# Optimization experiments

Hardware: AMD Instinct MI355X
Metric: run time of the kernel (lower is better)

Reference implementation:

```python
import jax, jax.numpy as jnp
import numpy as np

B, N, FIN = 64, 128, 768
NFEAT, NHID, NHEADS, NCLASS = 1024, 512, 8, 512
ALPHA = 0.2
NEG_E = -9e15
NEG_S = -9e10


def setup_inputs():
    rng = np.random.RandomState(0)
    x = rng.randn(B, N, FIN).astype(np.float32)
    offset_mapping = np.zeros((B, N, 2), dtype=np.int32)
    attention_mask = np.zeros((B, N), dtype=np.float32)
    tag = np.zeros((B, N), dtype=np.float32)
    for b in range(B):
        pos, k, groups = 1, 0, 0
        n_words = int(rng.randint(30, 60))
        for _ in range(n_words):
            wl = int(rng.randint(1, 4))
            if k + wl > 120:
                break
            for _t in range(wl):
                offset_mapping[b, k] = (pos, pos + 2)  # contiguous inside word
                pos += 2
                k += 1
            pos += 1  # 1-char gap => word boundary: end == next_start - 1
            groups += 1
        groups -= 1  # last word is never closed (matches torch loop semantics)
        attention_mask[b, :groups] = 1.0
        tag[b, :groups] = (rng.rand(groups) > 0.1).astype(np.float32)
        tag[b, 0] = 1.0
    adj = (rng.rand(B, N, N) < 0.3).astype(np.float32)
    adj = np.clip(adj + np.eye(N, dtype=np.float32)[None], 0.0, 1.0)
    s = 0.02
    p = {
        'Wg_w': s * rng.randn(FIN, NFEAT), 'Wg_b': np.zeros(NFEAT),
        'hW_w': s * rng.randn(NHEADS, NFEAT, NHID), 'hW_b': np.zeros((NHEADS, NHID)),
        'ha_w': s * rng.randn(NHEADS, 2 * NHID), 'ha_b': np.zeros(NHEADS),
        'oW_w': s * rng.randn(NHID * NHEADS, NCLASS), 'oW_b': np.zeros(NCLASS),
        'oa_w': s * rng.randn(2 * NCLASS), 'oa_b': np.zeros(()),
        'fin_w': s * rng.randn(NCLASS, 1), 'fin_b': np.zeros(1),
    }
    inp = {
        'x': jnp.asarray(x), 'tag': jnp.asarray(tag),
        'offset_mapping': jnp.asarray(offset_mapping),
        'attention_mask': jnp.asarray(attention_mask), 'adj': jnp.asarray(adj),
    }
    for kk, vv in p.items():
        inp[kk] = jnp.asarray(np.asarray(vv, dtype=np.float32))
    return inp


def _group_pool(x, offs):
    # Vectorized form of the offset-grouped mean pooling loop.
    zero = (offs[:, :, 0] == 0) & (offs[:, :, 1] == 0)  # padding rows
    fz = jnp.argmax(zero, axis=1)                       # first padding row (break)
    pos = jnp.arange(N)
    valid = pos[None, :] < fz[:, None]
    nxt_start = jnp.concatenate([offs[:, 1:, 0], jnp.zeros((offs.shape[0], 1), offs.dtype)], axis=1)
    boundary = valid & (offs[:, :, 1] == nxt_start - 1)
    bi = boundary.astype(jnp.int32)
    cs = jnp.cumsum(bi, axis=1)
    seg = cs - bi                 # exclusive cumsum: group id per token
    G = cs[:, -1]                 # number of closed groups per row

    def per(xb, segb, bb):
        sums = jax.ops.segment_sum(xb, segb, num_segments=N + 1)[:N]
        cnts = jax.ops.segment_sum(jnp.ones((N,), xb.dtype), segb, num_segments=N + 1)[:N]
        ends = jax.ops.segment_sum((jnp.arange(N) + 1) * bb, segb, num_segments=N + 1)[:N]
        return sums, cnts, ends

    sums, cnts, ends = jax.vmap(per)(x, seg, bi)
    g = jnp.arange(N)[None, :]
    gv = g < G[:, None]
    x_off = jnp.where(gv[..., None], sums / jnp.maximum(cnts, 1.0)[..., None], 0.0)
    starts = jnp.concatenate([jnp.zeros((offs.shape[0], 1), jnp.int32), ends[:, :-1]], axis=1)
    starts = jnp.where(gv, starts, 0)
    ends = jnp.where(gv, ends, 0)
    return x_off, jnp.stack([starts, ends], axis=-1)  # [B,N,F_in], [B,N,2]


def _expand_row(fix):
    # Flatten [start,end) ranges in order until the first [0,0] row; rest = arange.
    zr = (fix[:, 0] == 0) & (fix[:, 1] == 0)
    fz = jnp.argmax(zr)
    valid = jnp.arange(N) < fz
    lens = jnp.where(valid, fix[:, 1] - fix[:, 0], 0)
    csum = jnp.cumsum(lens)
    excl = csum - lens
    total = csum[-1]
    l = jnp.arange(N)
    k = jnp.clip(jnp.searchsorted(csum, l, side='right'), 0, N - 1)
    val = fix[k, 0] + (l - excl[k])
    return jnp.where(l < total, val, l)


def _scores(x_off, tag, attention_mask, adj, Wg_w, Wg_b, hW_w, hW_b, ha_w, ha_b, oW_w, oW_b, oa_w, oa_b, fin_w, fin_b):
    xw = x_off @ Wg_w + Wg_b                                    # [B,N,NFEAT]
    h = jnp.einsum('bnf,hfo->bhno', xw, hW_w) + hW_b[None, :, None, :]
    # e_ij = leakyrelu(a1.h_i + a2.h_j + b): decomposition of a([h_i||h_j])
    e = jax.nn.leaky_relu(
        jnp.einsum('bhno,ho->bhn', h, ha_w[:, :NHID])[:, :, :, None]
        + jnp.einsum('bhno,ho->bhn', h, ha_w[:, NHID:])[:, :, None, :]
        + ha_b[None, :, None, None], ALPHA)
    att = jax.nn.softmax(jnp.where(adj[:, None, :, :] > 0, e, NEG_E), axis=-1)
    x1 = jax.nn.elu(jnp.einsum('bhij,bhjo->bhio', att, h))
    x1 = x1.transpose(0, 2, 1, 3).reshape(x1.shape[0], N, NHEADS * NHID)
    h2 = x1 @ oW_w + oW_b
    e2 = jax.nn.leaky_relu((h2 @ oa_w[:NCLASS])[:, :, None]
                           + (h2 @ oa_w[NCLASS:])[:, None, :] + oa_b, ALPHA)
    att2 = jax.nn.softmax(jnp.where(adj > 0, e2, NEG_E), axis=-1)
    x2 = jax.nn.elu(jnp.einsum('bij,bjo->bio', att2, h2))
    logits = (x2 @ fin_w + fin_b)[..., 0]                        # [B,N]
    m = jnp.where(tag > 0, attention_mask, 0.0)
    sc = jax.nn.softmax(jnp.where(m > 0, logits * m, NEG_S), axis=1)
    summary = m.sum(axis=1)
    ii = (jnp.arange(N, 0, -1).astype(jnp.float32)[None, :] / summary[:, None]) * m
    ii = jax.nn.softmax(jnp.where(m > 0, ii, NEG_S), axis=1)
    return sc + ii


def reference(x, tag, offset_mapping, attention_mask, adj, Wg_w, Wg_b, hW_w, hW_b, ha_w, ha_b, oW_w, oW_b, oa_w, oa_b, fin_w, fin_b):
    x_off, index_group = _group_pool(x, offset_mapping)
    sc = _scores(x_off, tag, attention_mask, adj, Wg_w, Wg_b, hW_w, hW_b, ha_w, ha_b, oW_w, oW_b, oa_w, oa_b, fin_w, fin_b)
    order = jnp.argsort(-sc, axis=1)  # jax argsort is stable; matches torch stable descending
    bidx = jnp.arange(sc.shape[0])[:, None]
    fix = index_group.at[bidx, order].set(index_group)  # scatter_(dim=1) with permutation index
    return jax.vmap(_expand_row)(fix)
```

## Files before the change

kernel.cpp:

```cpp
#include <hip/hip_runtime.h>
#include <cstddef>
#include <cstdint>

#define B_ 64
#define N_ 128
#define FIN_ 768
#define NEG_E_ (-9.0e15f)
#define NEG_S_ (-9.0e10f)
#define CHUNK_ 16

typedef unsigned short u16;
typedef unsigned int u32;
typedef float f32x4 __attribute__((ext_vector_type(4)));
typedef short s16x8 __attribute__((ext_vector_type(8)));
typedef u16 u16x4 __attribute__((ext_vector_type(4)));
typedef u16 u16x2 __attribute__((ext_vector_type(2)));

__device__ __forceinline__ u16 f2bf(float x) {
  u32 u = __float_as_uint(x);
  return (u16)((u + 0x7fffu + ((u >> 16) & 1u)) >> 16);
}
__device__ __forceinline__ float b2f(u16 h) {
  return __uint_as_float(((u32)h) << 16);
}

__global__ __launch_bounds__(256) void group_pool_kernel(
    const float* __restrict__ x, const int* __restrict__ offs,
    u16* __restrict__ xoh, u16* __restrict__ xol, int* __restrict__ ig)
{
  const int b = blockIdx.x;
  const int fc = blockIdx.y;
  const int tid = threadIdx.x;
  __shared__ int o0[N_ + 1], o1[N_];
  __shared__ int bi[N_], cs[N_];
  __shared__ int st[N_], en[N_];
  __shared__ float invlen[N_];
  __shared__ int fzs;

  if (tid < N_) {
    o0[tid] = offs[(b * N_ + tid) * 2 + 0];
    o1[tid] = offs[(b * N_ + tid) * 2 + 1];
  }
  if (tid == 0) { o0[N_] = 0; fzs = N_; }
  __syncthreads();
  if (tid < N_ && o0[tid] == 0 && o1[tid] == 0) atomicMin(&fzs, tid);
  __syncthreads();
  const int fz = fzs;
  if (tid < N_) {
    int nxt = o0[tid + 1];
    bi[tid] = (tid < fz && o1[tid] == nxt - 1) ? 1 : 0;
    cs[tid] = bi[tid];
  }
  __syncthreads();
  for (int d = 1; d < N_; d <<= 1) {
    int v = 0;
    if (tid < N_ && tid >= d) v = cs[tid - d];
    __syncthreads();
    if (tid < N_) cs[tid] += v;
    __syncthreads();
  }
  if (tid < N_ && bi[tid]) en[cs[tid] - 1] = tid + 1;
  __syncthreads();
  const int G = cs[N_ - 1];
  if (tid < G) {
    int s = tid ? en[tid - 1] : 0;
    st[tid] = s;
    invlen[tid] = 1.0f / (float)(en[tid] - s);
  }
  __syncthreads();
  if (fc == 0 && tid < N_) {
    int g = tid;
    ig[(b * N_ + g) * 2 + 0] = (g < G) ? st[g] : 0;
    ig[(b * N_ + g) * 2 + 1] = (g < G) ? en[g] : 0;
  }

  const int f = fc * 128 + (tid & 63) * 2;
  const float* xb = x + (size_t)b * N_ * FIN_ + f;
  for (int g = tid >> 6; g < N_; g += 4) {
    u16 h0 = 0, h1 = 0, l0 = 0, l1 = 0;
    if (g < G) {
      int s = st[g], e = en[g];
      float s0 = 0.0f, s1 = 0.0f;
      for (int k = s; k < e; ++k) {
        float2 v = *(const float2*)(xb + (size_t)k * FIN_);
        s0 += v.x; s1 += v.y;
      }
      float il = invlen[g];
      float m0 = s0 * il, m1 = s1 * il;
      h0 = f2bf(m0); l0 = f2bf(m0 - b2f(h0));
      h1 = f2bf(m1); l1 = f2bf(m1 - b2f(h1));
    }
    size_t oo = ((size_t)b * N_ + g) * FIN_ + f;
    u16x2 hv = {h0, h1}, lv = {l0, l1};
    *(u16x2*)(xoh + oo) = hv;
    *(u16x2*)(xol + oo) = lv;
  }
}

__global__ __launch_bounds__(256) void pack_wgT(
    const float* __restrict__ w, u16* __restrict__ th, u16* __restrict__ tl)
{
  __shared__ float t[32][33];
  const int k0 = blockIdx.x * 32, n0 = blockIdx.y * 32;
  const int r = threadIdx.x >> 3;
  const int c = (threadIdx.x & 7) * 4;
  float4 v = *(const float4*)(w + (size_t)(k0 + r) * 1024 + n0 + c);
  t[r][c] = v.x; t[r][c + 1] = v.y; t[r][c + 2] = v.z; t[r][c + 3] = v.w;
  __syncthreads();
  u16x4 hv, lv;
#pragma unroll
  for (int i = 0; i < 4; ++i) {
    float xv = t[c + i][r];
    u16 h = f2bf(xv);
    hv[i] = h; lv[i] = f2bf(xv - b2f(h));
  }
  size_t dst = (size_t)(n0 + r) * 768 + k0 + c;
  *(u16x4*)(th + dst) = hv;
  *(u16x4*)(tl + dst) = lv;
}
__global__ __launch_bounds__(256) void pack_hwT(
    const float* __restrict__ w, u16* __restrict__ th, u16* __restrict__ tl)
{
  __shared__ float t[32][33];
  const int o0 = blockIdx.x * 32, f0 = blockIdx.y * 32, hd = blockIdx.z;
  const int r = threadIdx.x >> 3;
  const int c = (threadIdx.x & 7) * 4;
  float4 v = *(const float4*)(w + ((size_t)hd * 1024 + f0 + r) * 512 + o0 + c);
  t[r][c] = v.x; t[r][c + 1] = v.y; t[r][c + 2] = v.z; t[r][c + 3] = v.w;
  __syncthreads();
  u16x4 hv, lv;
#pragma unroll
  for (int i = 0; i < 4; ++i) {
    float xv = t[c + i][r];
    u16 h = f2bf(xv);
    hv[i] = h; lv[i] = f2bf(xv - b2f(h));
  }
  size_t dst = ((size_t)hd * 512 + o0 + r) * 1024 + f0 + c;
  *(u16x4*)(th + dst) = hv;
  *(u16x4*)(tl + dst) = lv;
}
__global__ __launch_bounds__(256) void pack_owT(
    const float* __restrict__ w, u16* __restrict__ th, u16* __restrict__ tl)
{
  __shared__ float t[32][33];
  const int k0 = blockIdx.x * 32, o0 = blockIdx.y * 32;
  const int r = threadIdx.x >> 3;
  const int c = (threadIdx.x & 7) * 4;
  float4 v = *(const float4*)(w + (size_t)(k0 + r) * 512 + o0 + c);
  t[r][c] = v.x; t[r][c + 1] = v.y; t[r][c + 2] = v.z; t[r][c + 3] = v.w;
  __syncthreads();
  u16x4 hv, lv;
#pragma unroll
  for (int i = 0; i < 4; ++i) {
    float xv = t[c + i][r];
    u16 h = f2bf(xv);
    hv[i] = h; lv[i] = f2bf(xv - b2f(h));
  }
  size_t dst = (size_t)(o0 + r) * 4096 + k0 + c;
  *(u16x4*)(th + dst) = hv;
  *(u16x4*)(tl + dst) = lv;
}

__global__ __launch_bounds__(256) void mfma_split_gemm(
    const u16* __restrict__ Ah, const u16* __restrict__ Al,
    const u16* __restrict__ Bh, const u16* __restrict__ Bl,
    const float* __restrict__ bias, int bias_mode,
    u16* __restrict__ Oh, u16* __restrict__ Ol, float* __restrict__ Of,
    int out_f32, int do_elu,
    int K, int lda, int ldb,
    long long Az, long long Bz,
    int msh, long long s_mb, int nsh, long long s_nb, long long s_n,
    long long zb_s, long long zh_s, int zH)
{
  __shared__ u16 As_h[128][40];
  __shared__ u16 As_l[128][40];
  __shared__ u16 Bs_h[128][40];
  __shared__ u16 Bs_l[128][40];
  const int tid = threadIdx.x;
  const int wave = tid >> 6, lane = tid & 63;
  const int wm = (wave >> 1) * 64, wn = (wave & 1) * 64;
  const int bn = blockIdx.x * 128, bm = blockIdx.y * 128;
  const int z = blockIdx.z;
  const u16* Ahb = Ah + (long long)z * Az;
  const u16* Alb = Al + (long long)z * Az;
  const u16* Bhb = Bh + (long long)z * Bz;
  const u16* Blb = Bl + (long long)z * Bz;
  const int lm = lane & 15, lq = lane >> 4;

  const int sr = tid >> 1;
  const int sc = (tid & 1) * 16;
  const size_t ga = (size_t)(bm + sr) * lda + sc;
  const size_t gb = (size_t)(bn + sr) * ldb + sc;

  f32x4 acc[4][4];
#pragma unroll
  for (int i = 0; i < 4; ++i)
#pragma unroll
    for (int j = 0; j < 4; ++j) acc[i][j] = (f32x4){0.0f, 0.0f, 0.0f, 0.0f};

  uint4 r0, r1, r2, r3, r4, r5, r6, r7;
  r0 = *(const uint4*)(Ahb + ga);
  r1 = *(const uint4*)(Ahb + ga + 8);
  r2 = *(const uint4*)(Alb + ga);
  r3 = *(const uint4*)(Alb + ga + 8);
  r4 = *(const uint4*)(Bhb + gb);
  r5 = *(const uint4*)(Bhb + gb + 8);
  r6 = *(const uint4*)(Blb + gb);
  r7 = *(const uint4*)(Blb + gb + 8);

  for (int k0 = 0; k0 < K; k0 += 32) {
    __syncthreads();
    *(uint4*)&As_h[sr][sc] = r0;
    *(uint4*)&As_h[sr][sc + 8] = r1;
    *(uint4*)&As_l[sr][sc] = r2;
    *(uint4*)&As_l[sr][sc + 8] = r3;
    *(uint4*)&Bs_h[sr][sc] = r4;
    *(uint4*)&Bs_h[sr][sc + 8] = r5;
    *(uint4*)&Bs_l[sr][sc] = r6;
    *(uint4*)&Bs_l[sr][sc + 8] = r7;
    __syncthreads();
    int kn = k0 + 32;
    if (kn < K) {
      r0 = *(const uint4*)(Ahb + ga + kn);
      r1 = *(const uint4*)(Ahb + ga + kn + 8);
      r2 = *(const uint4*)(Alb + ga + kn);
      r3 = *(const uint4*)(Alb + ga + kn + 8);
      r4 = *(const uint4*)(Bhb + gb + kn);
      r5 = *(const uint4*)(Bhb + gb + kn + 8);
      r6 = *(const uint4*)(Blb + gb + kn);
      r7 = *(const uint4*)(Blb + gb + kn + 8);
    }
    s16x8 fa_h[4], fa_l[4], fb_h[4], fb_l[4];
#pragma unroll
    for (int t = 0; t < 4; ++t) {
      fa_h[t] = *(const s16x8*)&As_h[wm + t * 16 + lm][lq * 8];
      fa_l[t] = *(const s16x8*)&As_l[wm + t * 16 + lm][lq * 8];
      fb_h[t] = *(const s16x8*)&Bs_h[wn + t * 16 + lm][lq * 8];
      fb_l[t] = *(const s16x8*)&Bs_l[wn + t * 16 + lm][lq * 8];
    }
#pragma unroll
    for (int i = 0; i < 4; ++i)
#pragma unroll
      for (int j = 0; j < 4; ++j) {
        acc[i][j] = __builtin_amdgcn_mfma_f32_16x16x32_bf16(fa_h[i], fb_h[j], acc[i][j], 0, 0, 0);
        acc[i][j] = __builtin_amdgcn_mfma_f32_16x16x32_bf16(fa_h[i], fb_l[j], acc[i][j], 0, 0, 0);
        acc[i][j] = __builtin_amdgcn_mfma_f32_16x16x32_bf16(fa_l[i], fb_h[j], acc[i][j], 0, 0, 0);
      }
  }

  __syncthreads();
  const long long zoff = (long long)(z / zH) * zb_s + (long long)(z % zH) * zh_s;
  const int mmask = (1 << msh) - 1;
  const int nmask = (1 << nsh) - 1;
  char* lds_raw = (char*)&As_h[0][0] + wave * 4608;
  const int rn = lane >> 2;
  const int rm = (lane & 3) * 16;

  if (out_f32) {
    float* slab = (float*)lds_raw;
#pragma unroll
    for (int j = 0; j < 4; ++j) {
#pragma unroll
      for (int i = 0; i < 4; ++i) {
        int mb = bm + wm + i * 16 + lq * 4;
        int n = bn + wn + j * 16 + lm;
        f32x4 v = acc[i][j];
        if (bias_mode == 1) v += bias[n];
        else if (bias_mode == 2) { f32x4 b4 = *(const f32x4*)&bias[mb]; v += b4; }
        if (do_elu) {
          v.x = v.x > 0.0f ? v.x : expm1f(v.x);
          v.y = v.y > 0.0f ? v.y : expm1f(v.y);
          v.z = v.z > 0.0f ? v.z : expm1f(v.z);
          v.w = v.w > 0.0f ? v.w : expm1f(v.w);
        }
        *(f32x4*)&slab[lm * 68 + i * 16 + lq * 4] = v;
      }
      __syncthreads();
      int n = bn + wn + j * 16 + rn;
      int mbase = bm + wm + rm;
      long long off = (long long)(mbase >> msh) * s_mb + (mbase & mmask)
                    + (long long)(n >> nsh) * s_nb + (long long)(n & nmask) * s_n + zoff;
      const float* src = &slab[rn * 68 + rm];
      f32x4 v0 = *(const f32x4*)(src + 0);
      f32x4 v1 = *(const f32x4*)(src + 4);
      f32x4 v2 = *(const f32x4*)(src + 8);
      f32x4 v3 = *(const f32x4*)(src + 12);
      *(f32x4*)(Of + off + 0)  = v0;
      *(f32x4*)(Of + off + 4)  = v1;
      *(f32x4*)(Of + off + 8)  = v2;
      *(f32x4*)(Of + off + 12) = v3;
      __syncthreads();
    }
  } else {
    u16* slab_h = (u16*)lds_raw;
    u16* slab_l = slab_h + 16 * 72;
#pragma unroll
    for (int j = 0; j < 4; ++j) {
#pragma unroll
      for (int i = 0; i < 4; ++i) {
        int mb = bm + wm + i * 16 + lq * 4;
        int n = bn + wn + j * 16 + lm;
        f32x4 v = acc[i][j];
        if (bias_mode == 1) v += bias[n];
        else if (bias_mode == 2) { f32x4 b4 = *(const f32x4*)&bias[mb]; v += b4; }
        if (do_elu) {
          v.x = v.x > 0.0f ? v.x : expm1f(v.x);
          v.y = v.y > 0.0f ? v.y : expm1f(v.y);
          v.z = v.z > 0.0f ? v.z : expm1f(v.z);
          v.w = v.w > 0.0f ? v.w : expm1f(v.w);
        }
        u16 h0 = f2bf(v.x), h1 = f2bf(v.y), h2 = f2bf(v.z), h3 = f2bf(v.w);
        u16x4 hv = {h0, h1, h2, h3};
        u16x4 lv = {f2bf(v.x - b2f(h0)), f2bf(v.y - b2f(h1)),
                    f2bf(v.z - b2f(h2)), f2bf(v.w - b2f(h3))};
        *(u16x4*)&slab_h[lm * 72 + i * 16 + lq * 4] = hv;
        *(u16x4*)&slab_l[lm * 72 + i * 16 + lq * 4] = lv;
      }
      __syncthreads();
      int n = bn + wn + j * 16 + rn;
      int mbase = bm + wm + rm;
      long long off = (long long)(mbase >> msh) * s_mb + (mbase & mmask)
                    + (long long)(n >> nsh) * s_nb + (long long)(n & nmask) * s_n + zoff;
      const u16* sh = &slab_h[rn * 72 + rm];
      const u16* sl = &slab_l[rn * 72 + rm];
      uint4 h0 = *(const uint4*)(sh + 0);
      uint4 h1 = *(const uint4*)(sh + 8);
      uint4 l0 = *(const uint4*)(sl + 0);
      uint4 l1 = *(const uint4*)(sl + 8);
      *(uint4*)(Oh + off + 0) = h0;
      *(uint4*)(Oh + off + 8) = h1;
      *(uint4*)(Ol + off + 0) = l0;
      *(uint4*)(Ol + off + 8) = l1;
      __syncthreads();
    }
  }
}

#define G8_BUF 49152

#define STAGE_A8(T) do { const int _t = (T); if (_t < nt) {                    \
    const int _q = _t % 3;                                                     \
    _Pragma("unroll")                                                          \
    for (int rg_ = 0; rg_ < 2; ++rg_)                                          \
      __builtin_amdgcn_global_load_lds(                                        \
          (const __attribute__((address_space(1))) void*)(gA +                 \
              (size_t)_t * 32 + (size_t)rg_ * 8 * lda),                        \
          (__attribute__((address_space(3))) void*)(ldsAd + _q * G8_BUF +      \
              rg_ * 1024),                                                     \
          16, 0, 0);                                                           \
  } } while (0)

#define STAGE_B8(T) do { const int _t = (T); if (_t < nt) {                    \
    const int _q = _t % 3;                                                     \
    _Pragma("unroll")                                                          \
    for (int rg_ = 0; rg_ < 4; ++rg_)                                          \
      __builtin_amdgcn_global_load_lds(                                        \
          (const __attribute__((address_space(1))) void*)(gB +                 \
              (size_t)_t * 32 + (size_t)rg_ * 8 * ldb),                        \
          (__attribute__((address_space(3))) void*)(ldsBd + _q * G8_BUF +      \
              rg_ * 1024),                                                     \
          16, 0, 0);                                                           \
  } } while (0)

__global__ __launch_bounds__(512, 2) void mfma_split_gemm8(
    const u16* __restrict__ Ah, const u16* __restrict__ Al,
    const u16* __restrict__ Bh, const u16* __restrict__ Bl,
    const float* __restrict__ bias, int bias_mode,
    u16* __restrict__ Oh, u16* __restrict__ Ol,
    int K, int lda, int ldb,
    int msh, long long s_mb, int nsh, long long s_nb, long long s_n)
{
  __shared__ __align__(128) char ldsb[3 * G8_BUF];
  const int tid = threadIdx.x;
  const int wave = tid >> 6, lane = tid & 63;
  const int wm = (wave >> 2) * 64, wn = (wave & 3) * 64;
  const int bn = blockIdx.x * 256, bm = blockIdx.y * 128;
  const int lm = lane & 15, lq = lane >> 4;
  const int nt = K >> 5;

  const int srow = lane >> 3;
  const int sl = (lane & 7) ^ srow;
  const int scol = (sl & 3) * 8;
  const u16* Asel = (sl < 4) ? Ah : Al;
  const u16* Bsel = (sl < 4) ? Bh : Bl;

  const u16* gA = Asel + (size_t)(bm + wave * 16 + srow) * lda + scol;
  const u16* gB = Bsel + (size_t)(bn + wave * 32 + srow) * ldb + scol;
  char* ldsAd = ldsb + wave * 2048;
  char* ldsBd = ldsb + 16384 + wave * 4096;

  const int hbyt = (lq ^ (lm & 7)) * 16;
  const int lbyt = hbyt ^ 64;

  f32x4 acc[4][4];
#pragma unroll
  for (int i = 0; i < 4; ++i)
#pragma unroll
    for (int j = 0; j < 4; ++j) acc[i][j] = (f32x4){0.0f, 0.0f, 0.0f, 0.0f};

  STAGE_A8(0); STAGE_B8(0);
  STAGE_A8(1); STAGE_B8(1);
  if (nt > 1) asm volatile("s_waitcnt vmcnt(6)" ::: "memory");
  else        asm volatile("s_waitcnt vmcnt(0)" ::: "memory");
  __builtin_amdgcn_s_barrier();
  __builtin_amdgcn_sched_barrier(0);

#pragma unroll 3
  for (int t = 0; t < nt; ++t) {
    const int q = t % 3;
    STAGE_A8(t + 2);
    STAGE_B8(t + 2);
    const char* Abase = ldsb + q * G8_BUF + (wm + lm) * 128;
    const char* Bbase = ldsb + q * G8_BUF + 16384 + (wn + lm) * 128;
    s16x8 fa[4][2], fb[4][2];
#pragma unroll
    for (int i = 0; i < 4; ++i) {
      fb[i][0] = *(const s16x8*)(Bbase + i * 2048 + hbyt);
      fb[i][1] = *(const s16x8*)(Bbase + i * 2048 + lbyt);
      fa[i][0] = *(const s16x8*)(Abase + i * 2048 + hbyt);
      fa[i][1] = *(const s16x8*)(Abase + i * 2048 + lbyt);
    }
    __builtin_amdgcn_s_setprio(1);
#pragma unroll
    for (int i = 0; i < 4; ++i)
#pragma unroll
      for (int j = 0; j < 4; ++j) {
        acc[i][j] = __builtin_amdgcn_mfma_f32_16x16x32_bf16(fa[i][0], fb[j][0], acc[i][j], 0, 0, 0);
        acc[i][j] = __builtin_amdgcn_mfma_f32_16x16x32_bf16(fa[i][0], fb[j][1], acc[i][j], 0, 0, 0);
        acc[i][j] = __builtin_amdgcn_mfma_f32_16x16x32_bf16(fa[i][1], fb[j][0], acc[i][j], 0, 0, 0);
      }
    __builtin_amdgcn_s_setprio(0);
    if (t + 1 < nt) {
      if (t + 2 < nt) asm volatile("s_waitcnt vmcnt(6)" ::: "memory");
      else            asm volatile("s_waitcnt vmcnt(0)" ::: "memory");
      __builtin_amdgcn_s_barrier();
      __builtin_amdgcn_sched_barrier(0);
    }
  }

  __syncthreads();
  const int mmask = (1 << msh) - 1;
  const int nmask = (1 << nsh) - 1;
  char* lds_raw = ldsb + wave * 4608;
  const int rn = lane >> 2;
  const int rm = (lane & 3) * 16;
  u16* slab_h = (u16*)lds_raw;
  u16* slab_l = slab_h + 16 * 72;
#pragma unroll
  for (int j = 0; j < 4; ++j) {
#pragma unroll
    for (int i = 0; i < 4; ++i) {
      int mb = bm + wm + i * 16 + lq * 4;
      int n = bn + wn + j * 16 + lm;
      f32x4 v = acc[i][j];
      if (bias_mode == 1) v += bias[n];
      else if (bias_mode == 2) { f32x4 b4 = *(const f32x4*)&bias[mb]; v += b4; }
      u16 h0 = f2bf(v.x), h1 = f2bf(v.y), h2 = f2bf(v.z), h3 = f2bf(v.w);
      u16x4 hv = {h0, h1, h2, h3};
      u16x4 lv = {f2bf(v.x - b2f(h0)), f2bf(v.y - b2f(h1)),
                  f2bf(v.z - b2f(h2)), f2bf(v.w - b2f(h3))};
      *(u16x4*)&slab_h[lm * 72 + i * 16 + lq * 4] = hv;
      *(u16x4*)&slab_l[lm * 72 + i * 16 + lq * 4] = lv;
    }
    __syncthreads();
    int n = bn + wn + j * 16 + rn;
    int mbase = bm + wm + rm;
    long long off = (long long)(mbase >> msh) * s_mb + (mbase & mmask)
                  + (long long)(n >> nsh) * s_nb + (long long)(n & nmask) * s_n;
    const u16* sh = &slab_h[rn * 72 + rm];
    const u16* slp = &slab_l[rn * 72 + rm];
    uint4 h0 = *(const uint4*)(sh + 0);
    uint4 h1 = *(const uint4*)(sh + 8);
    uint4 l0 = *(const uint4*)(slp + 0);
    uint4 l1 = *(const uint4*)(slp + 8);
    *(uint4*)(Oh + off + 0) = h0;
    *(uint4*)(Oh + off + 8) = h1;
    *(uint4*)(Ol + off + 0) = l0;
    *(uint4*)(Ol + off + 8) = l1;
    __syncthreads();
  }
}

__global__ __launch_bounds__(256) void reduce4_bias(
    const float* __restrict__ ps, const float* __restrict__ bias,
    float* __restrict__ h2T, int col0)
{
  int base = (blockIdx.x * 256 + threadIdx.x) * 4;
  int o = base >> 11, m = base & 2047;
  f32x4 v = *(const f32x4*)(ps + base);
  v += *(const f32x4*)(ps + base + 1048576);
  v += *(const f32x4*)(ps + base + 2097152);
  v += *(const f32x4*)(ps + base + 3145728);
  v += bias[o];
  *(f32x4*)(h2T + (size_t)o * 8192 + col0 + m) = v;
}

__global__ __launch_bounds__(512) void dot_pairs_hT(
    const u16* __restrict__ hTh, const u16* __restrict__ hTl,
    const float* __restrict__ W,
    float* __restrict__ esrc, float* __restrict__ edst)
{
  int bh = blockIdx.x;
  int head = bh & 7;
  int tid = threadIdx.x;
  int os = tid >> 7, i = tid & 127;
  const u16* ph = hTh + (size_t)bh * 65536 + (size_t)os * 16384 + i;
  const u16* pl = hTl + (size_t)bh * 65536 + (size_t)os * 16384 + i;
  const float* w1 = W + head * 1024 + os * 128;
  float s1 = 0.0f, s2 = 0.0f;
#pragma unroll 8
  for (int o = 0; o < 128; ++o) {
    float hv = b2f(ph[o * 128]) + b2f(pl[o * 128]);
    s1 = fmaf(hv, w1[o], s1);
    s2 = fmaf(hv, w1[512 + o], s2);
  }
  __shared__ float sh1[4][128], sh2[4][128];
  sh1[os][i] = s1;
  sh2[os][i] = s2;
  __syncthreads();
  if (os == 0) {
    esrc[bh * 128 + i] = sh1[0][i] + sh1[1][i] + sh1[2][i] + sh1[3][i];
    edst[bh * 128 + i] = sh2[0][i] + sh2[1][i] + sh2[2][i] + sh2[3][i];
  }
}

__global__ __launch_bounds__(512) void dot_pairs_h2T(
    const float* __restrict__ h2T, const float* __restrict__ oa,
    float* __restrict__ e2s, float* __restrict__ e2d)
{
  int b = blockIdx.x;
  int tid = threadIdx.x;
  int os = tid >> 7, i = tid & 127;
  const float* hb = h2T + (size_t)os * 128 * 8192 + b * 128 + i;
  const float* oa1 = oa + os * 128;
  float s1 = 0.0f, s2 = 0.0f;
#pragma unroll 8
  for (int o = 0; o < 128; ++o) {
    float hv = hb[(size_t)o * 8192];
    s1 = fmaf(hv, oa1[o], s1);
    s2 = fmaf(hv, oa1[512 + o], s2);
  }
  __shared__ float sh1[4][128], sh2[4][128];
  sh1[os][i] = s1;
  sh2[os][i] = s2;
  __syncthreads();
  if (os == 0) {
    e2s[b * 128 + i] = sh1[0][i] + sh1[1][i] + sh1[2][i] + sh1[3][i];
    e2d[b * 128 + i] = sh2[0][i] + sh2[1][i] + sh2[2][i] + sh2[3][i];
  }
}

__global__ __launch_bounds__(64) void edge_softmax_kernel(
    const float* __restrict__ esrc, const float* __restrict__ edst,
    const float* __restrict__ bias, const float* __restrict__ adj,
    float* __restrict__ attf, u16* __restrict__ atth, u16* __restrict__ attl,
    int H, int split)
{
  int row = blockIdx.x;
  int lane = threadIdx.x;
  int i = row & 127;
  int bh = row >> 7;
  int hd = bh % H;
  int b = bh / H;
  float es = esrc[row] + bias[hd];
  const float* adjr = adj + ((size_t)b * N_ + i) * N_;
  const float* edr = edst + (size_t)bh * N_;
  float v[2];
#pragma unroll
  for (int t = 0; t < 2; ++t) {
    int j = lane + t * 64;
    float e = es + edr[j];
    e = (e >= 0.0f) ? e : 0.2f * e;
    v[t] = (adjr[j] > 0.0f) ? e : NEG_E_;
  }
  float mx = fmaxf(v[0], v[1]);
  for (int off = 32; off; off >>= 1) mx = fmaxf(mx, __shfl_xor(mx, off));
  float e0 = expf(v[0] - mx), e1 = expf(v[1] - mx);
  float sm = e0 + e1;
  for (int off = 32; off; off >>= 1) sm += __shfl_xor(sm, off);
  float inv = 1.0f / sm;
  float p0 = e0 * inv, p1 = e1 * inv;
  size_t base = (size_t)row * N_;
  if (split) {
    u16 h0 = f2bf(p0), h1 = f2bf(p1);
    atth[base + lane] = h0;
    attl[base + lane] = f2bf(p0 - b2f(h0));
    atth[base + lane + 64] = h1;
    attl[base + lane + 64] = f2bf(p1 - b2f(h1));
  } else {
    attf[base + lane] = p0;
    attf[base + lane + 64] = p1;
  }
}

__global__ __launch_bounds__(256) void bgemm_elu_bt_f32(
    const float* __restrict__ A, const float* __restrict__ BT,
    float* __restrict__ C)
{
  __shared__ float As[16][64];
  __shared__ float Bs[16][68];
  const int tid = threadIdx.x;
  const int tm = blockIdx.x >> 3, tn = blockIdx.x & 7;
  const int bm = tm * 64, bn = tn * 64;
  const int b = blockIdx.y;
  const float* Ab = A + (size_t)b * 16384;
  const float* BTb = BT + (size_t)b * 128;
  const int ty = tid >> 4, tx = tid & 15;
  const int ar = tid >> 2, ac = (tid & 3) * 4;
  float acc[4][4];
#pragma unroll
  for (int i = 0; i < 4; ++i)
#pragma unroll
    for (int j = 0; j < 4; ++j) acc[i][j] = 0.0f;

  for (int k0 = 0; k0 < 128; k0 += 16) {
    float4 av = *(const float4*)(Ab + (size_t)(bm + ar) * 128 + k0 + ac);
    float4 bv = *(const float4*)(BTb + (size_t)(bn + ar) * 8192 + k0 + ac);
    __syncthreads();
    As[ac + 0][ar] = av.x; As[ac + 1][ar] = av.y; As[ac + 2][ar] = av.z; As[ac + 3][ar] = av.w;
    Bs[ac + 0][ar] = bv.x; Bs[ac + 1][ar] = bv.y; Bs[ac + 2][ar] = bv.z; Bs[ac + 3][ar] = bv.w;
    __syncthreads();
#pragma unroll
    for (int kk = 0; kk < 16; ++kk) {
      float a[4], bb[4];
      *(float4*)a  = *(const float4*)&As[kk][ty * 4];
      *(float4*)bb = *(const float4*)&Bs[kk][tx * 4];
#pragma unroll
      for (int i = 0; i < 4; ++i)
#pragma unroll
        for (int j = 0; j < 4; ++j)
          acc[i][j] = fmaf(a[i], bb[j], acc[i][j]);
    }
  }
#pragma unroll
  for (int i = 0; i < 4; ++i) {
    int row = b * 128 + bm + ty * 4 + i;
    float4 v;
    v.x = acc[i][0] > 0.0f ? acc[i][0] : expm1f(acc[i][0]);
    v.y = acc[i][1] > 0.0f ? acc[i][1] : expm1f(acc[i][1]);
    v.z = acc[i][2] > 0.0f ? acc[i][2] : expm1f(acc[i][2]);
    v.w = acc[i][3] > 0.0f ? acc[i][3] : expm1f(acc[i][3]);
    *(float4*)(C + (size_t)row * 512 + bn + tx * 4) = v;
  }
}

__global__ __launch_bounds__(256) void logits_kernel(
    const float* __restrict__ X, const float* __restrict__ w,
    const float* __restrict__ bptr, float* __restrict__ out, int R)
{
  int wv = (blockIdx.x * 256 + threadIdx.x) >> 6;
  int lane = threadIdx.x & 63;
  if (wv >= R) return;
  const float* xr = X + (size_t)wv * 512;
  float s = 0.0f;
#pragma unroll
  for (int i = 0; i < 8; ++i) {
    int c = lane + i * 64;
    s = fmaf(xr[c], w[c], s);
  }
  for (int off = 32; off; off >>= 1) s += __shfl_down(s, off);
  if (lane == 0) out[wv] = s + bptr[0];
}

__global__ __launch_bounds__(128) void finalize_kernel(
    const float* __restrict__ logits, const float* __restrict__ tag,
    const float* __restrict__ amask, const int* __restrict__ ig,
    int* __restrict__ out)
{
  const int b = blockIdx.x, tid = threadIdx.x;
  __shared__ float red[N_];
  __shared__ float scs[N_];
  __shared__ int fs[N_], fe[N_], lens[N_], csum[N_];
  __shared__ int redi[N_];

  float lg = logits[b * N_ + tid];
  float tg = tag[b * N_ + tid];
  float am = amask[b * N_ + tid];
  float m = (tg > 0.0f) ? am : 0.0f;

  float in1 = (m > 0.0f) ? lg * m : NEG_S_;
  red[tid] = in1; __syncthreads();
  for (int s = 64; s > 0; s >>= 1) { if (tid < s) red[tid] = fmaxf(red[tid], red[tid + s]); __syncthreads(); }
  float M1 = red[0]; __syncthreads();
  float e1 = expf(in1 - M1);
  red[tid] = e1; __syncthreads();
  for (int s = 64; s > 0; s >>= 1) { if (tid < s) red[tid] += red[tid + s]; __syncthreads(); }
  float S1 = red[0]; __syncthreads();
  float sc = e1 / S1;

  red[tid] = m; __syncthreads();
  for (int s = 64; s > 0; s >>= 1) { if (tid < s) red[tid] += red[tid + s]; __syncthreads(); }
  float SM = red[0]; __syncthreads();

  float in2 = (m > 0.0f) ? ((float)(N_ - tid) / SM) * m : NEG_S_;
  red[tid] = in2; __syncthreads();
  for (int s = 64; s > 0; s >>= 1) { if (tid < s) red[tid] = fmaxf(red[tid], red[tid + s]); __syncthreads(); }
  float M2 = red[0]; __syncthreads();
  float e2 = expf(in2 - M2);
  red[tid] = e2; __syncthreads();
  for (int s = 64; s > 0; s >>= 1) { if (tid < s) red[tid] += red[tid + s]; __syncthreads(); }
  float S2 = red[0]; __syncthreads();
  float ii = e2 / S2;

  scs[tid] = sc + ii;
  __syncthreads();

  float si = scs[tid];
  int rank = 0;
  for (int j = 0; j < N_; ++j) {
    float sj = scs[j];
    rank += (sj > si) || (sj == si && j < tid);
  }
  fs[tid] = ig[(b * N_ + rank) * 2 + 0];
  fe[tid] = ig[(b * N_ + rank) * 2 + 1];
  __syncthreads();

  redi[tid] = (fs[tid] == 0 && fe[tid] == 0) ? tid : N_;
  __syncthreads();
  for (int s = 64; s > 0; s >>= 1) { if (tid < s) redi[tid] = min(redi[tid], redi[tid + s]); __syncthreads(); }
  int fz = redi[0]; __syncthreads();
  lens[tid] = (tid < fz) ? (fe[tid] - fs[tid]) : 0;
  __syncthreads();
  if (tid == 0) {
    int r = 0;
    for (int k = 0; k < N_; ++k) { r += lens[k]; csum[k] = r; }
  }
  __syncthreads();
  int total = csum[N_ - 1];
  int l = tid;
  int k = 0;
  while (k < N_ && csum[k] <= l) ++k;
  if (k > N_ - 1) k = N_ - 1;
  int val = fs[k] + (l - (csum[k] - lens[k]));
  out[b * N_ + l] = (l < total) ? val : l;
}

extern "C" void kernel_launch(void* const* d_in, const int* in_sizes, int n_in,
                              void* d_out, int out_size, void* d_ws, size_t ws_size,
                              hipStream_t stream)
{
  const float* x     = (const float*)d_in[0];
  const float* tag   = (const float*)d_in[1];
  const int*   offs  = (const int*)  d_in[2];
  const float* amask = (const float*)d_in[3];
  const float* adj   = (const float*)d_in[4];
  const float* Wg_w  = (const float*)d_in[5];
  const float* Wg_b  = (const float*)d_in[6];
  const float* hW_w  = (const float*)d_in[7];
  const float* hW_b  = (const float*)d_in[8];
  const float* ha_w  = (const float*)d_in[9];
  const float* ha_b  = (const float*)d_in[10];
  const float* oW_w  = (const float*)d_in[11];
  const float* oW_b  = (const float*)d_in[12];
  const float* oa_w  = (const float*)d_in[13];
  const float* oa_b  = (const float*)d_in[14];
  const float* fin_w = (const float*)d_in[15];
  const float* fin_b = (const float*)d_in[16];
  int* out = (int*)d_out;

  char* ws = (char*)d_ws;
  size_t o = 0;
  int* ig     = (int*)(ws + o);  o += 131072;
  u16* WgT_h  = (u16*)(ws + o);  o += 1572864;
  u16* WgT_l  = (u16*)(ws + o);  o += 1572864;
  u16* hWT_h  = (u16*)(ws + o);  o += 8388608;
  u16* hWT_l  = (u16*)(ws + o);  o += 8388608;
  u16* oWT_h  = (u16*)(ws + o);  o += 4194304;
  u16* oWT_l  = (u16*)(ws + o);  o += 4194304;
  float* h2T  = (float*)(ws + o); o += 16777216;
  float* esrc = (float*)(ws + o); o += 65536;
  float* edst = (float*)(ws + o); o += 65536;
  float* e2s  = (float*)(ws + o); o += 32768;
  float* e2d  = (float*)(ws + o); o += 32768;
  float* lgts = (float*)(ws + o); o += 32768;
  u16* xw_h   = (u16*)(ws + o);  o += 16777216;
  u16* xw_l   = (u16*)(ws + o);  o += 16777216;
  char* pool  = ws + o;          o += 75497472;

  u16* xoff_h = (u16*)(pool + 0);
  u16* xoff_l = (u16*)(pool + 12582912);
  u16* hT_h   = (u16*)(pool + 0);
  u16* hT_l   = (u16*)(pool + 16777216);
  u16* x1_h   = (u16*)(pool + 33554432);
  u16* x1_l   = (u16*)(pool + 50331648);
  u16* att_h  = (u16*)(pool + 67108864);
  u16* att_l  = (u16*)(pool + 71303168);
  float* ps   = (float*)(pool + 0);
  float* att2 = (float*)(pool + 0);
  float* x2   = (float*)(pool + 4194304);

  pack_wgT<<<dim3(24, 32), 256, 0, stream>>>(Wg_w, WgT_h, WgT_l);
  pack_hwT<<<dim3(16, 32, 8), 256, 0, stream>>>(hW_w, hWT_h, hWT_l);
  pack_owT<<<dim3(128, 16), 256, 0, stream>>>(oW_w, oWT_h, oWT_l);

  group_pool_kernel<<<dim3(B_, 6), 256, 0, stream>>>(x, offs, xoff_h, xoff_l, ig);

  mfma_split_gemm8<<<dim3(32, 8), 512, 0, stream>>>(
      WgT_h, WgT_l, xoff_h, xoff_l, Wg_b, 2,
      xw_h, xw_l,
      768, 768, 768,
      10, 0, 13, 0, 1024);

  for (int b0 = 0; b0 < B_; b0 += CHUNK_) {
    mfma_split_gemm8<<<dim3(16, 16), 512, 0, stream>>>(
        xw_h + (size_t)b0 * 131072, xw_l + (size_t)b0 * 131072,
        hWT_h, hWT_l, hW_b, 1,
        hT_h, hT_l,
        1024, 1024, 1024,
        7, 524288, 9, 65536, 128);

    dot_pairs_hT<<<CHUNK_ * 8, 512, 0, stream>>>(hT_h, hT_l, ha_w, esrc, edst);
    edge_softmax_kernel<<<CHUNK_ * 8 * 128, 64, 0, stream>>>(
        esrc, edst, ha_b, adj + (size_t)b0 * 16384, nullptr, att_h, att_l, 8, 1);

    mfma_split_gemm<<<dim3(1, 4, CHUNK_ * 8), 256, 0, stream>>>(
        hT_h, hT_l, att_h, att_l, nullptr, 0,
        x1_h, x1_l, nullptr, 0, 1,
        128, 128, 128, 65536, 16384,
        9, 0, 7, 0, 4096, 524288, 512, 8);

    mfma_split_gemm<<<dim3(4, 16, 4), 256, 0, stream>>>(
        x1_h, x1_l, oWT_h, oWT_l, nullptr, 0,
        nullptr, nullptr, ps, 1, 0,
        1024, 4096, 4096, 1024, 1024,
        13, 0, 9, 0, 2048, 0, 1048576, 4);
    reduce4_bias<<<1024, 256, 0, stream>>>(ps, oW_b, h2T, b0 * 128);
  }

  dot_pairs_h2T<<<64, 512, 0, stream>>>(h2T, oa_w, e2s, e2d);
  edge_softmax_kernel<<<8192, 64, 0, stream>>>(e2s, e2d, oa_b, adj,
      att2, nullptr, nullptr, 1, 0);
  bgemm_elu_bt_f32<<<dim3(16, 64), 256, 0, stream>>>(att2, h2T, x2);

  logits_kernel<<<2048, 256, 0, stream>>>(x2, fin_w, fin_b, lgts, 8192);
  finalize_kernel<<<B_, 128, 0, stream>>>(lgts, tag, amask, ig, out);
}
```

Before: 802.1 us.

## Route output-projection GEMM through split-K gemm8 and batch edge softmax rows

Adds a split-K z-dimension and an fp32 output path to the 512-thread triple-buffered gemm8 kernel. The per-chunk output projection moves from the older mfma_split_gemm with 4 K-splits to gemm8 with 8 K-splits of 512, and the reduce kernel now sums 8 partials. Edge softmax packs four rows per 256-thread block to cut block count. The gemm8 inner loop splits the B-fragment loads and MFMAs into two halves separated by sched barriers to overlap LDS reads with math. The trade-offs are more partial-sum traffic and a doubled ps buffer footprint.

```diff
diff --git a/kernel.cpp b/kernel.cpp
--- a/kernel.cpp
+++ b/kernel.cpp
@@ -367,14 +367,17 @@
     const u16* __restrict__ Bh, const u16* __restrict__ Bl,
     const float* __restrict__ bias, int bias_mode,
     u16* __restrict__ Oh, u16* __restrict__ Ol,
+    float* __restrict__ Of, int out_f32,
     int K, int lda, int ldb,
-    int msh, long long s_mb, int nsh, long long s_nb, long long s_n)
+    int msh, long long s_mb, int nsh, long long s_nb, long long s_n,
+    int zKS, long long zOs)
 {
   __shared__ __align__(128) char ldsb[3 * G8_BUF];
   const int tid = threadIdx.x;
   const int wave = tid >> 6, lane = tid & 63;
   const int wm = (wave >> 2) * 64, wn = (wave & 3) * 64;
   const int bn = blockIdx.x * 256, bm = blockIdx.y * 128;
+  const int z = blockIdx.z;
   const int lm = lane & 15, lq = lane >> 4;
   const int nt = K >> 5;
 
@@ -384,8 +387,8 @@
   const u16* Asel = (sl < 4) ? Ah : Al;
   const u16* Bsel = (sl < 4) ? Bh : Bl;
 
-  const u16* gA = Asel + (size_t)(bm + wave * 16 + srow) * lda + scol;
-  const u16* gB = Bsel + (size_t)(bn + wave * 32 + srow) * ldb + scol;
+  const u16* gA = Asel + (size_t)(bm + wave * 16 + srow) * lda + scol + (size_t)z * zKS;
+  const u16* gB = Bsel + (size_t)(bn + wave * 32 + srow) * ldb + scol + (size_t)z * zKS;
   char* ldsAd = ldsb + wave * 2048;
   char* ldsBd = ldsb + 16384 + wave * 4096;
 
@@ -415,16 +418,37 @@
     s16x8 fa[4][2], fb[4][2];
 #pragma unroll
     for (int i = 0; i < 4; ++i) {
-      fb[i][0] = *(const s16x8*)(Bbase + i * 2048 + hbyt);
-      fb[i][1] = *(const s16x8*)(Bbase + i * 2048 + lbyt);
       fa[i][0] = *(const s16x8*)(Abase + i * 2048 + hbyt);
       fa[i][1] = *(const s16x8*)(Abase + i * 2048 + lbyt);
     }
+#pragma unroll
+    for (int j = 0; j < 2; ++j) {
+      fb[j][0] = *(const s16x8*)(Bbase + j * 2048 + hbyt);
+      fb[j][1] = *(const s16x8*)(Bbase + j * 2048 + lbyt);
+    }
+    __builtin_amdgcn_sched_barrier(0);
+#pragma unroll
+    for (int j = 2; j < 4; ++j) {
+      fb[j][0] = *(const s16x8*)(Bbase + j * 2048 + hbyt);
+      fb[j][1] = *(const s16x8*)(Bbase + j * 2048 + lbyt);
+    }
+    __builtin_amdgcn_sched_barrier(0);
     __builtin_amdgcn_s_setprio(1);
 #pragma unroll
-    for (int i = 0; i < 4; ++i)
-#pragma unroll
-      for (int j = 0; j < 4; ++j) {
+    for (int j = 0; j < 2; ++j)
+#pragma unroll
+      for (int i = 0; i < 4; ++i) {
+        acc[i][j] = __builtin_amdgcn_mfma_f32_16x16x32_bf16(fa[i][0], fb[j][0], acc[i][j], 0, 0, 0);
+        acc[i][j] = __builtin_amdgcn_mfma_f32_16x16x32_bf16(fa[i][0], fb[j][1], acc[i][j], 0, 0, 0);
+        acc[i][j] = __builtin_amdgcn_mfma_f32_16x16x32_bf16(fa[i][1], fb[j][0], acc[i][j], 0, 0, 0);
+      }
+    __builtin_amdgcn_s_setprio(0);
+    __builtin_amdgcn_sched_barrier(0);
+    __builtin_amdgcn_s_setprio(1);
+#pragma unroll
+    for (int j = 2; j < 4; ++j)
+#pragma unroll
+      for (int i = 0; i < 4; ++i) {
         acc[i][j] = __builtin_amdgcn_mfma_f32_16x16x32_bf16(fa[i][0], fb[j][0], acc[i][j], 0, 0, 0);
         acc[i][j] = __builtin_amdgcn_mfma_f32_16x16x32_bf16(fa[i][0], fb[j][1], acc[i][j], 0, 0, 0);
         acc[i][j] = __builtin_amdgcn_mfma_f32_16x16x32_bf16(fa[i][1], fb[j][0], acc[i][j], 0, 0, 0);
@@ -439,58 +463,91 @@
   }
 
   __syncthreads();
+  const long long zoff = (long long)z * zOs;
   const int mmask = (1 << msh) - 1;
   const int nmask = (1 << nsh) - 1;
   char* lds_raw = ldsb + wave * 4608;
   const int rn = lane >> 2;
   const int rm = (lane & 3) * 16;
-  u16* slab_h = (u16*)lds_raw;
-  u16* slab_l = slab_h + 16 * 72;
-#pragma unroll
-  for (int j = 0; j < 4; ++j) {
-#pragma unroll
-    for (int i = 0; i < 4; ++i) {
-      int mb = bm + wm + i * 16 + lq * 4;
-      int n = bn + wn + j * 16 + lm;
-      f32x4 v = acc[i][j];
-      if (bias_mode == 1) v += bias[n];
-      else if (bias_mode == 2) { f32x4 b4 = *(const f32x4*)&bias[mb]; v += b4; }
-      u16 h0 = f2bf(v.x), h1 = f2bf(v.y), h2 = f2bf(v.z), h3 = f2bf(v.w);
-      u16x4 hv = {h0, h1, h2, h3};
-      u16x4 lv = {f2bf(v.x - b2f(h0)), f2bf(v.y - b2f(h1)),
-                  f2bf(v.z - b2f(h2)), f2bf(v.w - b2f(h3))};
-      *(u16x4*)&slab_h[lm * 72 + i * 16 + lq * 4] = hv;
-      *(u16x4*)&slab_l[lm * 72 + i * 16 + lq * 4] = lv;
-    }
-    __syncthreads();
-    int n = bn + wn + j * 16 + rn;
-    int mbase = bm + wm + rm;
-    long long off = (long long)(mbase >> msh) * s_mb + (mbase & mmask)
-                  + (long long)(n >> nsh) * s_nb + (long long)(n & nmask) * s_n;
-    const u16* sh = &slab_h[rn * 72 + rm];
-    const u16* slp = &slab_l[rn * 72 + rm];
-    uint4 h0 = *(const uint4*)(sh + 0);
-    uint4 h1 = *(const uint4*)(sh + 8);
-    uint4 l0 = *(const uint4*)(slp + 0);
-    uint4 l1 = *(const uint4*)(slp + 8);
-    *(uint4*)(Oh + off + 0) = h0;
-    *(uint4*)(Oh + off + 8) = h1;
-    *(uint4*)(Ol + off + 0) = l0;
-    *(uint4*)(Ol + off + 8) = l1;
-    __syncthreads();
-  }
-}
-
-__global__ __launch_bounds__(256) void reduce4_bias(
+
+  if (out_f32) {
+    float* slab = (float*)lds_raw;
+#pragma unroll
+    for (int j = 0; j < 4; ++j) {
+#pragma unroll
+      for (int i = 0; i < 4; ++i) {
+        int mb = bm + wm + i * 16 + lq * 4;
+        int n = bn + wn + j * 16 + lm;
+        f32x4 v = acc[i][j];
+        if (bias_mode == 1) v += bias[n];
+        else if (bias_mode == 2) { f32x4 b4 = *(const f32x4*)&bias[mb]; v += b4; }
+        *(f32x4*)&slab[lm * 68 + i * 16 + lq * 4] = v;
+      }
+      __syncthreads();
+      int n = bn + wn + j * 16 + rn;
+      int mbase = bm + wm + rm;
+      long long off = (long long)(mbase >> msh) * s_mb + (mbase & mmask)
+                    + (long long)(n >> nsh) * s_nb + (long long)(n & nmask) * s_n + zoff;
+      const float* src = &slab[rn * 68 + rm];
+      f32x4 v0 = *(const f32x4*)(src + 0);
+      f32x4 v1 = *(const f32x4*)(src + 4);
+      f32x4 v2 = *(const f32x4*)(src + 8);
+      f32x4 v3 = *(const f32x4*)(src + 12);
+      *(f32x4*)(Of + off + 0)  = v0;
+      *(f32x4*)(Of + off + 4)  = v1;
+      *(f32x4*)(Of + off + 8)  = v2;
+      *(f32x4*)(Of + off + 12) = v3;
+      __syncthreads();
+    }
+  } else {
+    u16* slab_h = (u16*)lds_raw;
+    u16* slab_l = slab_h + 16 * 72;
+#pragma unroll
+    for (int j = 0; j < 4; ++j) {
+#pragma unroll
+      for (int i = 0; i < 4; ++i) {
+        int mb = bm + wm + i * 16 + lq * 4;
+        int n = bn + wn + j * 16 + lm;
+        f32x4 v = acc[i][j];
+        if (bias_mode == 1) v += bias[n];
+        else if (bias_mode == 2) { f32x4 b4 = *(const f32x4*)&bias[mb]; v += b4; }
+        u16 h0 = f2bf(v.x), h1 = f2bf(v.y), h2 = f2bf(v.z), h3 = f2bf(v.w);
+        u16x4 hv = {h0, h1, h2, h3};
+        u16x4 lv = {f2bf(v.x - b2f(h0)), f2bf(v.y - b2f(h1)),
+                    f2bf(v.z - b2f(h2)), f2bf(v.w - b2f(h3))};
+        *(u16x4*)&slab_h[lm * 72 + i * 16 + lq * 4] = hv;
+        *(u16x4*)&slab_l[lm * 72 + i * 16 + lq * 4] = lv;
+      }
+      __syncthreads();
+      int n = bn + wn + j * 16 + rn;
+      int mbase = bm + wm + rm;
+      long long off = (long long)(mbase >> msh) * s_mb + (mbase & mmask)
+                    + (long long)(n >> nsh) * s_nb + (long long)(n & nmask) * s_n + zoff;
+      const u16* sh = &slab_h[rn * 72 + rm];
+      const u16* slp = &slab_l[rn * 72 + rm];
+      uint4 h0 = *(const uint4*)(sh + 0);
+      uint4 h1 = *(const uint4*)(sh + 8);
+      uint4 l0 = *(const uint4*)(slp + 0);
+      uint4 l1 = *(const uint4*)(slp + 8);
+      *(uint4*)(Oh + off + 0) = h0;
+      *(uint4*)(Oh + off + 8) = h1;
+      *(uint4*)(Ol + off + 0) = l0;
+      *(uint4*)(Ol + off + 8) = l1;
+      __syncthreads();
+    }
+  }
+}
+
+__global__ __launch_bounds__(256) void reduce8_bias(
     const float* __restrict__ ps, const float* __restrict__ bias,
     float* __restrict__ h2T, int col0)
 {
   int base = (blockIdx.x * 256 + threadIdx.x) * 4;
   int o = base >> 11, m = base & 2047;
   f32x4 v = *(const f32x4*)(ps + base);
-  v += *(const f32x4*)(ps + base + 1048576);
-  v += *(const f32x4*)(ps + base + 2097152);
-  v += *(const f32x4*)(ps + base + 3145728);
+#pragma unroll
+  for (int s = 1; s < 8; ++s)
+    v += *(const f32x4*)(ps + base + (size_t)s * 1048576);
   v += bias[o];
   *(f32x4*)(h2T + (size_t)o * 8192 + col0 + m) = v;
 }
@@ -550,14 +607,14 @@
   }
 }
 
-__global__ __launch_bounds__(64) void edge_softmax_kernel(
+__global__ __launch_bounds__(256) void edge_softmax_kernel(
     const float* __restrict__ esrc, const float* __restrict__ edst,
     const float* __restrict__ bias, const float* __restrict__ adj,
     float* __restrict__ attf, u16* __restrict__ atth, u16* __restrict__ attl,
     int H, int split)
 {
-  int row = blockIdx.x;
-  int lane = threadIdx.x;
+  int row = blockIdx.x * 4 + (threadIdx.x >> 6);
+  int lane = threadIdx.x & 63;
   int i = row & 127;
   int bh = row >> 7;
   int hd = bh % H;
@@ -795,22 +852,22 @@
 
   group_pool_kernel<<<dim3(B_, 6), 256, 0, stream>>>(x, offs, xoff_h, xoff_l, ig);
 
-  mfma_split_gemm8<<<dim3(32, 8), 512, 0, stream>>>(
+  mfma_split_gemm8<<<dim3(32, 8, 1), 512, 0, stream>>>(
       WgT_h, WgT_l, xoff_h, xoff_l, Wg_b, 2,
-      xw_h, xw_l,
+      xw_h, xw_l, nullptr, 0,
       768, 768, 768,
-      10, 0, 13, 0, 1024);
+      10, 0, 13, 0, 1024, 0, 0);
 
   for (int b0 = 0; b0 < B_; b0 += CHUNK_) {
-    mfma_split_gemm8<<<dim3(16, 16), 512, 0, stream>>>(
+    mfma_split_gemm8<<<dim3(16, 16, 1), 512, 0, stream>>>(
         xw_h + (size_t)b0 * 131072, xw_l + (size_t)b0 * 131072,
         hWT_h, hWT_l, hW_b, 1,
-        hT_h, hT_l,
+        hT_h, hT_l, nullptr, 0,
         1024, 1024, 1024,
-        7, 524288, 9, 65536, 128);
+        7, 524288, 9, 65536, 128, 0, 0);
 
     dot_pairs_hT<<<CHUNK_ * 8, 512, 0, stream>>>(hT_h, hT_l, ha_w, esrc, edst);
-    edge_softmax_kernel<<<CHUNK_ * 8 * 128, 64, 0, stream>>>(
+    edge_softmax_kernel<<<CHUNK_ * 8 * 32, 256, 0, stream>>>(
         esrc, edst, ha_b, adj + (size_t)b0 * 16384, nullptr, att_h, att_l, 8, 1);
 
     mfma_split_gemm<<<dim3(1, 4, CHUNK_ * 8), 256, 0, stream>>>(
@@ -819,16 +876,16 @@
         128, 128, 128, 65536, 16384,
         9, 0, 7, 0, 4096, 524288, 512, 8);
 
-    mfma_split_gemm<<<dim3(4, 16, 4), 256, 0, stream>>>(
+    mfma_split_gemm8<<<dim3(2, 16, 8), 512, 0, stream>>>(
         x1_h, x1_l, oWT_h, oWT_l, nullptr, 0,
-        nullptr, nullptr, ps, 1, 0,
-        1024, 4096, 4096, 1024, 1024,
-        13, 0, 9, 0, 2048, 0, 1048576, 4);
-    reduce4_bias<<<1024, 256, 0, stream>>>(ps, oW_b, h2T, b0 * 128);
+        nullptr, nullptr, ps, 1,
+        512, 4096, 4096,
+        13, 0, 9, 0, 2048, 512, 1048576);
+    reduce8_bias<<<1024, 256, 0, stream>>>(ps, oW_b, h2T, b0 * 128);
   }
 
   dot_pairs_h2T<<<64, 512, 0, stream>>>(h2T, oa_w, e2s, e2d);
-  edge_softmax_kernel<<<8192, 64, 0, stream>>>(e2s, e2d, oa_b, adj,
+  edge_softmax_kernel<<<2048, 256, 0, stream>>>(e2s, e2d, oa_b, adj,
       att2, nullptr, nullptr, 1, 0);
   bgemm_elu_bt_f32<<<dim3(16, 64), 256, 0, stream>>>(att2, h2T, x2);
 
```

Result: faster. 775.6 us (-3.3%).
